# Performance work log

Measured on AMD Instinct MI355X. Metric: run time of the kernel, lower is better.

## Reference

```python
import jax, jax.numpy as jnp
import numpy as np

SHRINK_THRES = 0.0025
R_THRES = 1.0
EPS = 1e-12


def setup_inputs() -> dict:
    key = jax.random.key(0)
    k1, k2 = jax.random.split(key)
    N, L, D = 16384, 4096, 1024  # samples, memory slots (lan_dim), fea_dim
    x = jax.random.normal(k1, (N, D), dtype=jnp.float32)
    stdv = 1.0 / np.sqrt(D)
    weight = jax.random.uniform(k2, (L, D), dtype=jnp.float32, minval=-stdv, maxval=stdv)
    return {"x": x, "weight": weight}


def reference(x, weight):
    # memory addressing: att = softmax(x @ W^T)  -> [N, L]
    att = jax.nn.softmax(x @ weight.T, axis=1)
    # hard_shrink_relu: relu(a - lambd) * a / (|a - lambd| + eps)
    shifted = att - SHRINK_THRES
    att = jax.nn.relu(shifted) * att / (jnp.abs(shifted) + EPS)
    # L1 normalize along dim 1 (F.normalize p=1, eps=1e-12)
    l1 = jnp.sum(jnp.abs(att), axis=1, keepdims=True)
    att = att / jnp.maximum(l1, EPS)
    # reconstruct from memory: [N, D]
    output = att @ weight
    # nearest landmark per sample (detached gather in original)
    ind = jnp.argmax(att, axis=1)                      # [N]
    nl = weight[ind]                                   # [N, D]
    # second-nearest: overwrite argmax slot with the row minimum, re-argmax
    rows = jnp.arange(att.shape[0])
    row_min = jnp.min(att, axis=1)
    att2 = att.at[rows, ind].set(row_min)
    ind2 = jnp.argmax(att2, axis=1)
    nl2 = weight[ind2]                                 # [N, D]
    # centroid-distance filter (original returns list of indices; we return a
    # jit-compatible boolean mask over samples instead)
    cen = jnp.mean(weight, axis=0)                     # [D]
    dist = jnp.sqrt(jnp.sum((x - cen) ** 2, axis=1))   # [N]
    col_mask = dist < R_THRES                          # [N] bool
    return (output, att, nl, nl2, col_mask)
```

## Files before the change

### kernel.cpp

```cpp
#include <hip/hip_runtime.h>
#include <cmath>

#define NS 16384
#define LS 4096
#define DF 1024
#define SHRINK_T 0.0025f
#define EPS_T 1e-12f

using f16 = _Float16;
using f16x4 = __attribute__((ext_vector_type(4))) _Float16;
using f16x8 = __attribute__((ext_vector_type(8))) _Float16;
using f32x16 = __attribute__((ext_vector_type(16))) float;

#define NSEG 64

__global__ void split_kernel(const float* __restrict__ src,
                             f16* __restrict__ hi, f16* __restrict__ lo, int n4) {
    int i = blockIdx.x * 256 + threadIdx.x;
    if (i >= n4) return;
    float4 v = reinterpret_cast<const float4*>(src)[i];
    f16x4 h, l;
    h[0] = (f16)v.x; h[1] = (f16)v.y; h[2] = (f16)v.z; h[3] = (f16)v.w;
    l[0] = (f16)(v.x - (float)h[0]);
    l[1] = (f16)(v.y - (float)h[1]);
    l[2] = (f16)(v.z - (float)h[2]);
    l[3] = (f16)(v.w - (float)h[3]);
    reinterpret_cast<f16x4*>(hi)[i] = h;
    reinterpret_cast<f16x4*>(lo)[i] = l;
}

__global__ void centroid_part_kernel(const float* __restrict__ w, float* __restrict__ part) {
    const int c = blockIdx.x * 256 + threadIdx.x;
    const int seg = blockIdx.y;
    const int l0 = seg * (LS / NSEG);
    float acc = 0.f;
    for (int l = 0; l < LS / NSEG; ++l)
        acc += w[(size_t)(l0 + l) * DF + c];
    part[(size_t)seg * DF + c] = acc;
}

__global__ void centroid_sum_kernel(const float* __restrict__ part, float* __restrict__ cen) {
    const int c = blockIdx.x * 256 + threadIdx.x;
    float acc = 0.f;
    for (int s = 0; s < NSEG; ++s) acc += part[(size_t)s * DF + c];
    cen[c] = acc * (1.0f / (float)LS);
}

#define BM 256
#define BN 128
#define BK 16
#define NKT (DF / BK)

#define GLOAD16(gptr, lptr)                                                    \
    __builtin_amdgcn_global_load_lds(                                          \
        (const __attribute__((address_space(1))) void*)(gptr),                 \
        (__attribute__((address_space(3))) void*)(lptr), 16, 0, 0)

__global__ __launch_bounds__(256, 2) void gemm_f16_kernel(
    const f16* __restrict__ xh, const f16* __restrict__ xl,
    const f16* __restrict__ wh, const f16* __restrict__ wl,
    float* __restrict__ S, int r0, int rowsChunk)
{
    __shared__ __align__(16) f16 Ah[2][BM * BK];
    __shared__ __align__(16) f16 Al[2][BM * BK];
    __shared__ __align__(16) f16 Bh[2][BN * BK];
    __shared__ __align__(16) f16 Bl[2][BN * BK];

    const int t = threadIdx.x;
    const int lane = t & 63;
    const int wv = t >> 6;
    const int rowBase = r0 + blockIdx.y * BM;
    const int colBase = blockIdx.x * BN;

    f32x16 acc[2][4];
#pragma unroll
    for (int m = 0; m < 2; ++m)
#pragma unroll
        for (int n = 0; n < 4; ++n)
#pragma unroll
            for (int j = 0; j < 16; ++j) acc[m][n][j] = 0.f;

    const int c32 = lane & 31;
    const int kh = lane >> 5;

    const int srow = t >> 1;
    const int sc = (t & 1) * 8;
    int ga0 = rowBase + srow;        if (ga0 >= NS) ga0 = NS - 1;
    int ga1 = rowBase + 128 + srow;  if (ga1 >= NS) ga1 = NS - 1;
    const size_t aoff0 = (size_t)ga0 * DF + sc;
    const size_t aoff1 = (size_t)ga1 * DF + sc;
    const size_t boff  = (size_t)(colBase + srow) * DF + sc;
    const int lbA0 = wv * 512;
    const int lbA1 = 2048 + wv * 512;
    const int lbB  = wv * 512;

#define STAGE(k0, b)                                      \
    do {                                                  \
        GLOAD16(xh + aoff0 + (k0), &Ah[b][lbA0]);         \
        GLOAD16(xl + aoff0 + (k0), &Al[b][lbA0]);         \
        GLOAD16(xh + aoff1 + (k0), &Ah[b][lbA1]);         \
        GLOAD16(xl + aoff1 + (k0), &Al[b][lbA1]);         \
        GLOAD16(wh + boff  + (k0), &Bh[b][lbB]);          \
        GLOAD16(wl + boff  + (k0), &Bl[b][lbB]);          \
    } while (0)

    const int baseA = (wv * 64 + c32) * BK + kh * 8;
    const int baseB = c32 * BK + kh * 8;

    STAGE(0, 0);

    for (int kt = 0; kt < NKT; ++kt) {
        const int b = kt & 1;
        __syncthreads();
        if (kt + 1 < NKT) STAGE((kt + 1) * BK, b ^ 1);

        f16x8 amh[2], aml[2], bnh[4], bnl[4];
#pragma unroll
        for (int m = 0; m < 2; ++m) {
            amh[m] = *(const f16x8*)&Ah[b][baseA + m * 32 * BK];
            aml[m] = *(const f16x8*)&Al[b][baseA + m * 32 * BK];
        }
#pragma unroll
        for (int n = 0; n < 4; ++n) {
            bnh[n] = *(const f16x8*)&Bh[b][baseB + n * 32 * BK];
            bnl[n] = *(const f16x8*)&Bl[b][baseB + n * 32 * BK];
        }
#pragma unroll
        for (int m = 0; m < 2; ++m)
#pragma unroll
            for (int n = 0; n < 4; ++n) {
                acc[m][n] = __builtin_amdgcn_mfma_f32_32x32x16_f16(amh[m], bnh[n], acc[m][n], 0, 0, 0);
                acc[m][n] = __builtin_amdgcn_mfma_f32_32x32x16_f16(amh[m], bnl[n], acc[m][n], 0, 0, 0);
                acc[m][n] = __builtin_amdgcn_mfma_f32_32x32x16_f16(aml[m], bnh[n], acc[m][n], 0, 0, 0);
            }
    }
#undef STAGE

#pragma unroll
    for (int m = 0; m < 2; ++m) {
        const int rb = blockIdx.y * BM + wv * 64 + m * 32 + 4 * kh;
#pragma unroll
        for (int n = 0; n < 4; ++n) {
            const int cc = colBase + n * 32 + c32;
#pragma unroll
            for (int reg = 0; reg < 16; ++reg) {
                const int rr = rb + (reg & 3) + 8 * (reg >> 2);
                if (rr < rowsChunk)
                    S[(size_t)rr * LS + cc] = acc[m][n][reg];
            }
        }
    }
}

__global__ __launch_bounds__(256) void pass2_kernel(
    const float* __restrict__ S, const float* __restrict__ x,
    const float* __restrict__ w, const float* __restrict__ cen,
    float* __restrict__ out, int r0)
{
    constexpr int T = 256;
    __shared__ __align__(16) float att_lds[LS];
    __shared__ float red[T];
    __shared__ int redi[T];

    const int t = threadIdx.x;
    const size_t row = (size_t)r0 + blockIdx.x;
    const float4* s4 = (const float4*)(S + (size_t)blockIdx.x * (size_t)LS);

    float* const out_output = out;
    float* const out_att  = out + (size_t)NS * DF;
    float* const out_nl   = out + (size_t)NS * DF + (size_t)NS * LS;
    float* const out_nl2  = out + (size_t)2 * NS * DF + (size_t)NS * LS;
    float* const out_mask = out + (size_t)3 * NS * DF + (size_t)NS * LS;

    float sv[16];
    float mx = -INFINITY;
#pragma unroll
    for (int i = 0; i < 4; ++i) {
        float4 v = s4[i * 256 + t];
        sv[i * 4 + 0] = v.x; sv[i * 4 + 1] = v.y;
        sv[i * 4 + 2] = v.z; sv[i * 4 + 3] = v.w;
        mx = fmaxf(mx, fmaxf(fmaxf(v.x, v.y), fmaxf(v.z, v.w)));
    }
    red[t] = mx;
    __syncthreads();
    for (int off = 128; off >= 1; off >>= 1) {
        if (t < off) red[t] = fmaxf(red[t], red[t + off]);
        __syncthreads();
    }
    const float m = red[0];
    __syncthreads();

    float zs = 0.f;
#pragma unroll
    for (int i = 0; i < 16; ++i) {
        sv[i] = expf(sv[i] - m);
        zs += sv[i];
    }
    red[t] = zs;
    __syncthreads();
    for (int off = 128; off >= 1; off >>= 1) {
        if (t < off) red[t] += red[t + off];
        __syncthreads();
    }
    const float Z = red[0];
    __syncthreads();

    float l1 = 0.f;
#pragma unroll
    for (int i = 0; i < 16; ++i) {
        float a = sv[i] / Z;
        float r = a - SHRINK_T;
        float v = (r > 0.f) ? (r * a) / (r + EPS_T) : 0.f;
        sv[i] = v;
        l1 += v;
    }
    red[t] = l1;
    __syncthreads();
    for (int off = 128; off >= 1; off >>= 1) {
        if (t < off) red[t] += red[t + off];
        __syncthreads();
    }
    const float nrm = fmaxf(red[0], EPS_T);
    __syncthreads();

    float bv = -INFINITY; int bi = LS;
    float mn = INFINITY;
    float4* const attl4 = (float4*)att_lds;
    float4* const att4o = (float4*)(out_att + row * LS);
#pragma unroll
    for (int i = 0; i < 4; ++i) {
        float4 vn4;
        vn4.x = sv[i * 4 + 0] / nrm; vn4.y = sv[i * 4 + 1] / nrm;
        vn4.z = sv[i * 4 + 2] / nrm; vn4.w = sv[i * 4 + 3] / nrm;
        sv[i * 4 + 0] = vn4.x; sv[i * 4 + 1] = vn4.y;
        sv[i * 4 + 2] = vn4.z; sv[i * 4 + 3] = vn4.w;
        attl4[i * 256 + t] = vn4;
        att4o[i * 256 + t] = vn4;
#pragma unroll
        for (int c = 0; c < 4; ++c) {
            const float v = sv[i * 4 + c];
            const int j = i * 1024 + 4 * t + c;
            if (v > bv) { bv = v; bi = j; }
            mn = fminf(mn, v);
        }
    }
    __syncthreads();

    red[t] = bv; redi[t] = bi;
    __syncthreads();
    for (int off = 128; off >= 1; off >>= 1) {
        if (t < off) {
            float ov = red[t + off]; int oi = redi[t + off];
            if (ov > red[t] || (ov == red[t] && oi < redi[t])) { red[t] = ov; redi[t] = oi; }
        }
        __syncthreads();
    }
    const int ind = redi[0];
    __syncthreads();

    red[t] = mn;
    __syncthreads();
    for (int off = 128; off >= 1; off >>= 1) {
        if (t < off) red[t] = fminf(red[t], red[t + off]);
        __syncthreads();
    }
    const float rowmin = red[0];
    __syncthreads();

    bv = -INFINITY; bi = LS;
#pragma unroll
    for (int i = 0; i < 4; ++i)
#pragma unroll
        for (int c = 0; c < 4; ++c) {
            const int j = i * 1024 + 4 * t + c;
            const float vv = (j == ind) ? rowmin : sv[i * 4 + c];
            if (vv > bv) { bv = vv; bi = j; }
        }
    red[t] = bv; redi[t] = bi;
    __syncthreads();
    for (int off = 128; off >= 1; off >>= 1) {
        if (t < off) {
            float ov = red[t + off]; int oi = redi[t + off];
            if (ov > red[t] || (ov == red[t] && oi < redi[t])) { red[t] = ov; redi[t] = oi; }
        }
        __syncthreads();
    }
    const int ind2 = redi[0];
    __syncthreads();

    const int lane = t & 63;
    float4 oa = {0.f, 0.f, 0.f, 0.f};
    for (int k0 = 0; k0 < LS; k0 += 64) {
        float av = att_lds[k0 + lane];
        unsigned long long msk = __ballot(av > 0.f);
        while (msk) {
            int b = __ffsll((unsigned long long)msk) - 1;
            msk &= msk - 1;
            float vv = att_lds[k0 + b];
            float4 wv4 = ((const float4*)(w + (size_t)(k0 + b) * DF))[t];
            oa.x = fmaf(vv, wv4.x, oa.x);
            oa.y = fmaf(vv, wv4.y, oa.y);
            oa.z = fmaf(vv, wv4.z, oa.z);
            oa.w = fmaf(vv, wv4.w, oa.w);
        }
    }
    ((float4*)(out_output + row * DF))[t] = oa;

    ((float4*)(out_nl  + row * DF))[t] = ((const float4*)(w + (size_t)ind  * DF))[t];
    ((float4*)(out_nl2 + row * DF))[t] = ((const float4*)(w + (size_t)ind2 * DF))[t];

    float4 xv = ((const float4*)(x + row * DF))[t];
    float4 cv = ((const float4*)cen)[t];
    float ds = 0.f;
    ds = fmaf(xv.x - cv.x, xv.x - cv.x, ds);
    ds = fmaf(xv.y - cv.y, xv.y - cv.y, ds);
    ds = fmaf(xv.z - cv.z, xv.z - cv.z, ds);
    ds = fmaf(xv.w - cv.w, xv.w - cv.w, ds);
    red[t] = ds;
    __syncthreads();
    for (int off = 128; off >= 1; off >>= 1) {
        if (t < off) red[t] += red[t + off];
        __syncthreads();
    }
    if (t == 0) {
        float dist = sqrtf(red[0]);
        out_mask[row] = (dist < 1.0f) ? 1.0f : 0.0f;
    }
}

extern "C" void kernel_launch(void* const* d_in, const int* in_sizes, int n_in,
                              void* d_out, int out_size, void* d_ws, size_t ws_size,
                              hipStream_t stream)
{
    const float* x = (const float*)d_in[0];
    const float* w = (const float*)d_in[1];
    float* out = (float*)d_out;

    float* cen = (float*)d_ws;
    float* part = cen + DF;
    f16* xh = (f16*)(part + (size_t)NSEG * DF);
    f16* xl = xh + (size_t)NS * DF;
    f16* wh = xl + (size_t)NS * DF;
    f16* wl = wh + (size_t)LS * DF;
    float* S = (float*)(wl + (size_t)LS * DF);

    const size_t head_bytes = sizeof(float) * (DF + (size_t)NSEG * DF)
                            + (size_t)2 * 2 * NS * DF + (size_t)2 * 2 * LS * DF;
    long cap_rows = (long)((ws_size - head_bytes) / (sizeof(float) * LS));
    if (cap_rows > NS) cap_rows = NS;
    if (cap_rows < 1) cap_rows = 1;
    int chunk = (cap_rows >= BM) ? (int)(cap_rows - (cap_rows % BM)) : (int)cap_rows;

    centroid_part_kernel<<<dim3(DF / 256, NSEG), 256, 0, stream>>>(w, part);
    centroid_sum_kernel<<<DF / 256, 256, 0, stream>>>(part, cen);
    split_kernel<<<(NS * DF / 4 + 255) / 256, 256, 0, stream>>>(x, xh, xl, NS * DF / 4);
    split_kernel<<<(LS * DF / 4 + 255) / 256, 256, 0, stream>>>(w, wh, wl, LS * DF / 4);

    for (int r0 = 0; r0 < NS; r0 += chunk) {
        int rows = (NS - r0 < chunk) ? (NS - r0) : chunk;
        dim3 grid((LS + BN - 1) / BN, (rows + BM - 1) / BM);
        gemm_f16_kernel<<<grid, 256, 0, stream>>>(xh, xl, wh, wl, S, r0, rows);
        pass2_kernel<<<rows, 256, 0, stream>>>(S, x, w, cen, out, r0);
    }
}
```

Baseline: 697.4 us.

## Restructure split-f16 GEMM into 256x256 tiles with a 4-stage async LDS pipeline

The GEMM tile grows from 256x128 to 256x256 and runs with 512 threads as eight waves arranged 2x4. The old double buffer with a full __syncthreads is replaced by a 4-deep ring of global-to-LDS loads, kept in flight by explicit vmcnt waits and raw s_barrier, plus s_setprio around the MFMA block. The aim is more data reuse per loaded tile and better hiding of load latency behind the three-pass f16 MFMA. The larger tile and deeper ring raise LDS and register use, and the clamp on the A row index is gone, so it relies on rows always being a multiple of 256.

```diff
diff --git a/kernel.cpp b/kernel.cpp
--- a/kernel.cpp
+++ b/kernel.cpp
@@ -47,101 +47,102 @@
 }
 
 #define BM 256
-#define BN 128
-#define BK 16
-#define NKT (DF / BK)
+#define BN 256
+#define NSL (DF / 16)
 
 #define GLOAD16(gptr, lptr)                                                    \
     __builtin_amdgcn_global_load_lds(                                          \
         (const __attribute__((address_space(1))) void*)(gptr),                 \
         (__attribute__((address_space(3))) void*)(lptr), 16, 0, 0)
 
-__global__ __launch_bounds__(256, 2) void gemm_f16_kernel(
+__global__ __launch_bounds__(512, 2) void gemm_f16_kernel(
     const f16* __restrict__ xh, const f16* __restrict__ xl,
     const f16* __restrict__ wh, const f16* __restrict__ wl,
     float* __restrict__ S, int r0, int rowsChunk)
 {
-    __shared__ __align__(16) f16 Ah[2][BM * BK];
-    __shared__ __align__(16) f16 Al[2][BM * BK];
-    __shared__ __align__(16) f16 Bh[2][BN * BK];
-    __shared__ __align__(16) f16 Bl[2][BN * BK];
+    __shared__ __align__(16) f16 lds[4][4][2][256][8];
 
     const int t = threadIdx.x;
     const int lane = t & 63;
     const int wv = t >> 6;
+    const int wvm = wv >> 2;
+    const int wvn = wv & 3;
     const int rowBase = r0 + blockIdx.y * BM;
     const int colBase = blockIdx.x * BN;
 
-    f32x16 acc[2][4];
-#pragma unroll
-    for (int m = 0; m < 2; ++m)
-#pragma unroll
-        for (int n = 0; n < 4; ++n)
+    f32x16 acc[4][2];
+#pragma unroll
+    for (int m = 0; m < 4; ++m)
+#pragma unroll
+        for (int n = 0; n < 2; ++n)
 #pragma unroll
             for (int j = 0; j < 16; ++j) acc[m][n][j] = 0.f;
 
     const int c32 = lane & 31;
     const int kh = lane >> 5;
 
-    const int srow = t >> 1;
-    const int sc = (t & 1) * 8;
-    int ga0 = rowBase + srow;        if (ga0 >= NS) ga0 = NS - 1;
-    int ga1 = rowBase + 128 + srow;  if (ga1 >= NS) ga1 = NS - 1;
-    const size_t aoff0 = (size_t)ga0 * DF + sc;
-    const size_t aoff1 = (size_t)ga1 * DF + sc;
-    const size_t boff  = (size_t)(colBase + srow) * DF + sc;
-    const int lbA0 = wv * 512;
-    const int lbA1 = 2048 + wv * 512;
-    const int lbB  = wv * 512;
-
-#define STAGE(k0, b)                                      \
-    do {                                                  \
-        GLOAD16(xh + aoff0 + (k0), &Ah[b][lbA0]);         \
-        GLOAD16(xl + aoff0 + (k0), &Al[b][lbA0]);         \
-        GLOAD16(xh + aoff1 + (k0), &Ah[b][lbA1]);         \
-        GLOAD16(xl + aoff1 + (k0), &Al[b][lbA1]);         \
-        GLOAD16(wh + boff  + (k0), &Bh[b][lbB]);          \
-        GLOAD16(wl + boff  + (k0), &Bl[b][lbB]);          \
+    const int prow = t & 255;
+    const int pplane = t >> 8;
+    const size_t asrc = (size_t)(rowBase + prow) * DF + pplane * 8;
+    const size_t bsrc = (size_t)(colBase + prow) * DF + pplane * 8;
+    const int dstoff = (t & 448) * 8;
+
+#define STAGE(j)                                                        \
+    do {                                                                \
+        const int _b = (j) & 3;                                         \
+        const int _k = (j) * 16;                                        \
+        GLOAD16(xh + asrc + _k, &lds[_b][0][0][0][0] + dstoff);         \
+        GLOAD16(xl + asrc + _k, &lds[_b][1][0][0][0] + dstoff);         \
+        GLOAD16(wh + bsrc + _k, &lds[_b][2][0][0][0] + dstoff);         \
+        GLOAD16(wl + bsrc + _k, &lds[_b][3][0][0][0] + dstoff);         \
     } while (0)
 
-    const int baseA = (wv * 64 + c32) * BK + kh * 8;
-    const int baseB = c32 * BK + kh * 8;
-
-    STAGE(0, 0);
-
-    for (int kt = 0; kt < NKT; ++kt) {
-        const int b = kt & 1;
-        __syncthreads();
-        if (kt + 1 < NKT) STAGE((kt + 1) * BK, b ^ 1);
-
-        f16x8 amh[2], aml[2], bnh[4], bnl[4];
-#pragma unroll
-        for (int m = 0; m < 2; ++m) {
-            amh[m] = *(const f16x8*)&Ah[b][baseA + m * 32 * BK];
-            aml[m] = *(const f16x8*)&Al[b][baseA + m * 32 * BK];
-        }
-#pragma unroll
-        for (int n = 0; n < 4; ++n) {
-            bnh[n] = *(const f16x8*)&Bh[b][baseB + n * 32 * BK];
-            bnl[n] = *(const f16x8*)&Bl[b][baseB + n * 32 * BK];
-        }
-#pragma unroll
-        for (int m = 0; m < 2; ++m)
-#pragma unroll
-            for (int n = 0; n < 4; ++n) {
+    STAGE(0); STAGE(1); STAGE(2);
+
+    for (int j = 0; j < NSL; ++j) {
+        const int b = j & 3;
+        if (j <= 61)      asm volatile("s_waitcnt vmcnt(8)" ::: "memory");
+        else if (j == 62) asm volatile("s_waitcnt vmcnt(4)" ::: "memory");
+        else              asm volatile("s_waitcnt vmcnt(0)" ::: "memory");
+        __builtin_amdgcn_sched_barrier(0);
+        __builtin_amdgcn_s_barrier();
+        __builtin_amdgcn_sched_barrier(0);
+
+        f16x8 amh[4], aml[4], bnh[2], bnl[2];
+#pragma unroll
+        for (int m = 0; m < 4; ++m) {
+            const int r = wvm * 128 + m * 32 + c32;
+            amh[m] = *(const f16x8*)&lds[b][0][kh][r][0];
+            aml[m] = *(const f16x8*)&lds[b][1][kh][r][0];
+        }
+#pragma unroll
+        for (int n = 0; n < 2; ++n) {
+            const int r = wvn * 64 + n * 32 + c32;
+            bnh[n] = *(const f16x8*)&lds[b][2][kh][r][0];
+            bnl[n] = *(const f16x8*)&lds[b][3][kh][r][0];
+        }
+
+        if (j <= 60) STAGE(j + 3);
+
+        __builtin_amdgcn_s_setprio(1);
+#pragma unroll
+        for (int m = 0; m < 4; ++m)
+#pragma unroll
+            for (int n = 0; n < 2; ++n) {
                 acc[m][n] = __builtin_amdgcn_mfma_f32_32x32x16_f16(amh[m], bnh[n], acc[m][n], 0, 0, 0);
                 acc[m][n] = __builtin_amdgcn_mfma_f32_32x32x16_f16(amh[m], bnl[n], acc[m][n], 0, 0, 0);
                 acc[m][n] = __builtin_amdgcn_mfma_f32_32x32x16_f16(aml[m], bnh[n], acc[m][n], 0, 0, 0);
             }
+        __builtin_amdgcn_s_setprio(0);
     }
 #undef STAGE
 
 #pragma unroll
-    for (int m = 0; m < 2; ++m) {
-        const int rb = blockIdx.y * BM + wv * 64 + m * 32 + 4 * kh;
-#pragma unroll
-        for (int n = 0; n < 4; ++n) {
-            const int cc = colBase + n * 32 + c32;
+    for (int m = 0; m < 4; ++m) {
+        const int rb = blockIdx.y * BM + wvm * 128 + m * 32 + 4 * kh;
+#pragma unroll
+        for (int n = 0; n < 2; ++n) {
+            const int cc = colBase + wvn * 64 + n * 32 + c32;
 #pragma unroll
             for (int reg = 0; reg < 16; ++reg) {
                 const int rr = rb + (reg & 3) + 8 * (reg >> 2);
@@ -359,7 +360,7 @@
     for (int r0 = 0; r0 < NS; r0 += chunk) {
         int rows = (NS - r0 < chunk) ? (NS - r0) : chunk;
         dim3 grid((LS + BN - 1) / BN, (rows + BM - 1) / BM);
-        gemm_f16_kernel<<<grid, 256, 0, stream>>>(xh, xl, wh, wl, S, r0, rows);
+        gemm_f16_kernel<<<grid, 512, 0, stream>>>(xh, xl, wh, wl, S, r0, rows);
         pass2_kernel<<<rows, 256, 0, stream>>>(S, x, w, cen, out, r0);
     }
 }
```

After: 742.6 us. 6.5% more time.
